# Performance work log

Hardware: AMD Instinct MI355X
Metric: run time of the kernel (lower is better)

## Reference

```python
import jax, jax.numpy as jnp
import numpy as np
import math

# --- static model config (mirrors FitTorch init args) ---
NATOMS = 2000
NNBR = 30            # neighbors per atom (regular neighlist)
NPAIRS = NATOMS * NNBR
NCONF = 8
APC = NATOMS // NCONF
NUM_RADIAL = 12
NUM_3BODY = 20
CUTOFF = 5.0
H1, H2 = 64, 32
DESC = NUM_RADIAL + NUM_3BODY


def setup_inputs() -> dict:
    key = jax.random.key(0)
    ks = jax.random.split(key, 12)
    # positions in a box
    x = jax.random.uniform(ks[0], (NATOMS, 3), jnp.float32, 0.0, 20.0)
    unique_i = jnp.repeat(jnp.arange(NATOMS, dtype=jnp.int32), NNBR)
    unique_j = jax.random.randint(ks[1], (NPAIRS,), 0, NATOMS, dtype=jnp.int32)
    # construct transform_x so every pair distance lies in (1.0, 0.95*cutoff)
    dirs = jax.random.normal(ks[2], (NPAIRS, 3), jnp.float32)
    dirs = dirs / jnp.linalg.norm(dirs, axis=1, keepdims=True)
    r = jax.random.uniform(ks[3], (NPAIRS, 1), jnp.float32, 1.0, 0.95 * CUTOFF)
    xneigh_target = x[unique_i] - dirs * r
    transform_x = xneigh_target - x[unique_j]
    neighlist = jnp.stack([unique_i, unique_j], axis=1)
    indices = unique_i // APC                      # config id per pair
    atoms_per_structure = jnp.full((NCONF,), APC, dtype=jnp.int32)
    types = jnp.zeros((NATOMS,), dtype=jnp.int32)
    # tiny pairwise MLP params (sigmoid hidden layers, linear output)
    def lin(k, fan_in, fan_out):
        return jax.random.normal(k, (fan_in, fan_out), jnp.float32) / np.sqrt(fan_in)
    W1 = lin(ks[4], DESC, H1); b1 = jnp.zeros((H1,), jnp.float32)
    W2 = lin(ks[5], H1, H2);   b2 = jnp.zeros((H2,), jnp.float32)
    W3 = lin(ks[6], H2, 1);    b3 = jnp.zeros((1,), jnp.float32)
    return {"x": x, "transform_x": transform_x, "neighlist": neighlist,
            "indices": indices, "atoms_per_structure": atoms_per_structure,
            "types": types, "unique_i": unique_i, "unique_j": unique_j,
            "W1": W1, "b1": b1, "W2": W2, "b2": b2, "W3": W3, "b3": b3}


def _energy(x, transform_x, indices, unique_i, unique_j, W1, b1, W2, b2, W3, b3, nconf):
    # gather + pairwise geometry
    xneigh = transform_x + x[unique_j]                      # [P,3]
    diff = x[unique_i] - xneigh                             # [P,3]
    rij = jnp.linalg.norm(diff, axis=1, keepdims=True)      # [P,1]
    u = diff / jnp.maximum(rij, 1e-12)                      # F.normalize
    # smooth cosine cutoff
    fc = 0.5 * (jnp.cos(jnp.pi * rij / CUTOFF) + 1.0)       # [P,1]
    # radial Bessel basis: fc * sqrt(2/c) * sin(n*pi*r/c) / r, n=1..R
    n = jnp.arange(1, NUM_RADIAL + 1, dtype=x.dtype)
    rbf = fc * jnp.sqrt(2.0 / CUTOFF) * jnp.sin(n * jnp.pi * rij / CUTOFF) / rij  # [P,R]
    # 3-body Gaussian descriptors over angles j-i-k (neighbors grouped per atom i)
    A, N, M = x.shape[0], NNBR, NUM_3BODY
    u3 = u.reshape(A, N, 3)
    fcn = fc.reshape(A, N)
    cos = jnp.einsum('apd,aqd->apq', u3, u3)                # [A,N,N] cos(theta)
    mu = jnp.linspace(-1.0, 1.0, M).astype(x.dtype)
    dmu = mu[1] - mu[0]
    eta = 1.0 / (2.0 * dmu * dmu)
    self_mask = 1.0 - jnp.eye(N, dtype=x.dtype)             # exclude k == j
    w = fcn[:, None, :] * self_mask[None]                   # [A,N,N] fc(r_ik) weights
    g = jnp.exp(-eta * (cos[..., None] - mu) ** 2)          # [A,N,N,M]
    d3 = jnp.einsum('apq,apqm->apm', w, g).reshape(A * N, M)
    # pairwise MLP -> pair energies, modulated by cutoff
    desc = jnp.concatenate([rbf, d3], axis=1)               # [P, DESC]
    h = jax.nn.sigmoid(desc @ W1 + b1)
    h = jax.nn.sigmoid(h @ W2 + b2)
    eij = (h @ W3 + b3) * fc                                # [P,1]
    # scatter pair energies to per-structure totals (index_add_)
    return jax.ops.segment_sum(eij[:, 0], indices, num_segments=nconf)


def reference(x, transform_x, neighlist, indices, atoms_per_structure, types,
              unique_i, unique_j, W1, b1, W2, b2, W3, b3):
    nconf = atoms_per_structure.shape[0]
    energy = _energy(x, transform_x, indices, unique_i, unique_j,
                     W1, b1, W2, b2, W3, b3, nconf)
    # forces = -d(sum of energies)/dx (grad_outputs = ones), as in torch.autograd.grad
    forces = -jax.grad(lambda xx: _energy(xx, transform_x, indices, unique_i, unique_j,
                                          W1, b1, W2, b2, W3, b3, nconf).sum())(x)
    return energy, forces
```

## Files before the change

kernel.cpp:

```cpp
#include <hip/hip_runtime.h>
#include <math.h>

#define NATOMS 2000
#define NNBR   30
#define NCONF  8
#define APC    250
#define NRAD   12
#define M3     20
#define H1N    64
#define H2N    32

#define MU(m) (-1.0f + (float)(m) * (2.0f / 19.0f))

typedef __attribute__((ext_vector_type(8))) short short8_t;
typedef __attribute__((ext_vector_type(4))) float f32x4;

__device__ __forceinline__ float sigmoidf(float v) {
    return 1.0f / (1.0f + __expf(-v));
}
__device__ __forceinline__ ushort f2bf(float f) {
    unsigned u = __float_as_uint(f);
    u += 0x7FFF + ((u >> 16) & 1);
    return (ushort)(u >> 16);
}
__device__ __forceinline__ float bf2f(ushort s) {
    return __uint_as_float(((unsigned)s) << 16);
}

extern "C" __global__ void __launch_bounds__(256)
fit_main(const float* __restrict__ x, const float* __restrict__ tx,
         const int* __restrict__ uj,
         const float* __restrict__ W1, const float* __restrict__ b1,
         const float* __restrict__ W2, const float* __restrict__ b2,
         const float* __restrict__ W3, const float* __restrict__ b3,
         float* __restrict__ gx, float* __restrict__ e_atom)
{
    const int tid  = threadIdx.x;
    const int lane = tid & 63;
    const int wid  = tid >> 6;
    const int atom = blockIdx.x;
    const int lr   = lane & 15;
    const int lg   = lane >> 4;

    __shared__ float  s_u[NNBR][4];
    __shared__ float  s_geo[NNBR][8];
    __shared__ int    s_j[NNBR];
    __shared__ __align__(16) float  s_desc[32 * 36];
    __shared__ __align__(16) ushort s_W1b[32 * 72];
    __shared__ __align__(16) ushort s_W2tb[32 * 72];
    __shared__ __align__(16) ushort s_h1b[32 * 72];
    __shared__ __align__(16) ushort s_gz2b[32 * 40];
    __shared__ __align__(16) float  s_gd[32 * 44];
    __shared__ float  s_outp[64];
    __shared__ float  s_red[32 * 5];

    const float k1  = 0.6283185307179586f;
    const float sq  = 0.6324555320336759f;
    const float eta = 45.125f;
    const float RHO = 0.36787944117144233f;
    const float C2  = -90.25f;

#pragma unroll
    for (int i = 0; i < 8; i++) {
        int idx = tid + 256 * i;
        s_W1b[(idx >> 6) * 72 + (idx & 63)] = f2bf(W1[idx]);
    }
#pragma unroll
    for (int i = 0; i < 8; i++) {
        int idx = tid + 256 * i;
        s_W2tb[(idx & 31) * 72 + (idx >> 5)] = f2bf(W2[idx]);
    }
    if (tid < NNBR) {
        int p = atom * NNBR + tid;
        int j = uj[p];
        float d0 = x[atom * 3 + 0] - x[j * 3 + 0] - tx[p * 3 + 0];
        float d1 = x[atom * 3 + 1] - x[j * 3 + 1] - tx[p * 3 + 1];
        float d2 = x[atom * 3 + 2] - x[j * 3 + 2] - tx[p * 3 + 2];
        float r = sqrtf(d0 * d0 + d1 * d1 + d2 * d2);
        float rinv = 1.0f / r;
        float sa, ca;
        __sincosf(k1 * r, &sa, &ca);
        float fc = 0.5f * (ca + 1.0f);
        s_u[tid][0] = d0 * rinv; s_u[tid][1] = d1 * rinv; s_u[tid][2] = d2 * rinv;
        s_geo[tid][0] = fc; s_geo[tid][1] = r; s_geo[tid][2] = rinv;
        s_geo[tid][3] = sa; s_geo[tid][4] = ca;
        s_j[tid] = j;
    }
    __syncthreads();

#pragma unroll 1
    for (int t = tid; t < NNBR * NRAD; t += 256) {
        int p = t / NRAD, n = t - p * NRAD;
        float s = __sinf((float)(n + 1) * k1 * s_geo[p][1]);
        s_desc[p * 36 + n] = s_geo[p][0] * sq * s * s_geo[p][2];
    }
    if (tid < 72) s_desc[30 * 36 + tid] = 0.f;
    if (tid < 240) {
        int p = tid >> 3, c = tid & 7;
        int q0 = (c < 6) ? 4 * c : 24 + 3 * (c - 6);
        int qn = (c < 6) ? 4 : 3;
        float up0 = s_u[p][0], up1 = s_u[p][1], up2 = s_u[p][2];
        float d3part[M3];
#pragma unroll
        for (int m = 0; m < M3; m++) d3part[m] = 0.f;
        for (int qq = 0; qq < qn; qq++) {
            int q = q0 + qq;
            float fq = (q == p) ? 0.f : s_geo[q][0];
            float cs = up0 * s_u[q][0] + up1 * s_u[q][1] + up2 * s_u[q][2];
            float E  = __expf(9.5f * cs);
            float Ei = __expf(-9.5f * cs);
            float t9 = cs - MU(9);
            float h9 = __expf(-eta * t9 * t9);
            float h = h9 * E, rr = E * RHO;
            d3part[10] = fmaf(fq, h, d3part[10]);
#pragma unroll
            for (int m = 11; m < 20; m++) {
                h *= rr; rr *= RHO;
                d3part[m] = fmaf(fq, h, d3part[m]);
            }
            h = h9; rr = RHO * Ei;
            d3part[9] = fmaf(fq, h, d3part[9]);
#pragma unroll
            for (int m = 8; m >= 0; m--) {
                h *= rr; rr *= RHO;
                d3part[m] = fmaf(fq, h, d3part[m]);
            }
        }
#pragma unroll
        for (int m = 0; m < M3; m++) {
            float v = d3part[m];
            v += __shfl_xor(v, 1);
            v += __shfl_xor(v, 2);
            v += __shfl_xor(v, 4);
            if (c == 0) s_desc[p * 36 + NRAD + m] = v;
        }
    }
    __syncthreads();

    {
        const int mt = wid & 1, ntb = (wid >> 1) * 2;
        short8_t a;
        {
            const float* dp = s_desc + (16 * mt + lr) * 36 + lg * 8;
            f32x4 v0 = *(const f32x4*)dp;
            f32x4 v1 = *(const f32x4*)(dp + 4);
            a[0] = (short)f2bf(v0[0]); a[1] = (short)f2bf(v0[1]);
            a[2] = (short)f2bf(v0[2]); a[3] = (short)f2bf(v0[3]);
            a[4] = (short)f2bf(v1[0]); a[5] = (short)f2bf(v1[1]);
            a[6] = (short)f2bf(v1[2]); a[7] = (short)f2bf(v1[3]);
        }
#pragma unroll
        for (int t = 0; t < 2; t++) {
            int nt = ntb + t;
            int col = 16 * nt + lr;
            short8_t b;
#pragma unroll
            for (int j = 0; j < 8; j++)
                b[j] = (short)s_W1b[(lg * 8 + j) * 72 + col];
            f32x4 c = {0.f, 0.f, 0.f, 0.f};
            c = __builtin_amdgcn_mfma_f32_16x16x32_bf16(a, b, c, 0, 0, 0);
            float b1v = b1[col];
#pragma unroll
            for (int rg = 0; rg < 4; rg++) {
                int p = 16 * mt + lg * 4 + rg;
                s_h1b[p * 72 + col] = f2bf(sigmoidf(c[rg] + b1v));
            }
        }
    }
    __syncthreads();

    {
        const int mt = wid & 1, nt = wid >> 1;
        f32x4 c = {0.f, 0.f, 0.f, 0.f};
#pragma unroll
        for (int kt = 0; kt < 2; kt++) {
            short8_t a = *(const short8_t*)&s_h1b[(16 * mt + lr) * 72 + kt * 32 + lg * 8];
            short8_t b = *(const short8_t*)&s_W2tb[(16 * nt + lr) * 72 + kt * 32 + lg * 8];
            c = __builtin_amdgcn_mfma_f32_16x16x32_bf16(a, b, c, 0, 0, 0);
        }
        int k2 = 16 * nt + lr;
        float b2v = b2[k2], w3v = W3[k2];
        float op[4];
#pragma unroll
        for (int rg = 0; rg < 4; rg++) {
            int p = 16 * mt + lg * 4 + rg;
            float s = sigmoidf(c[rg] + b2v);
            op[rg] = s * w3v;
            float g = (p < NNBR) ? s_geo[p][0] * w3v * s * (1.f - s) : 0.f;
            s_gz2b[p * 40 + k2] = f2bf(g);
        }
#pragma unroll
        for (int rg = 0; rg < 4; rg++) {
            op[rg] += __shfl_xor(op[rg], 1);
            op[rg] += __shfl_xor(op[rg], 2);
            op[rg] += __shfl_xor(op[rg], 4);
            op[rg] += __shfl_xor(op[rg], 8);
        }
        if (lr == 0) {
#pragma unroll
            for (int rg = 0; rg < 4; rg++)
                s_outp[nt * 32 + 16 * mt + lg * 4 + rg] = op[rg];
        }
    }
    __syncthreads();

    {
        const int mt = wid & 1, ntb = (wid >> 1) * 2;
        short8_t a = *(const short8_t*)&s_gz2b[(16 * mt + lr) * 40 + lg * 8];
#pragma unroll
        for (int t = 0; t < 2; t++) {
            int nt = ntb + t;
            int hcol = 16 * nt + lr;
            short8_t b;
#pragma unroll
            for (int j = 0; j < 8; j++)
                b[j] = (short)s_W2tb[(lg * 8 + j) * 72 + hcol];
            f32x4 c = {0.f, 0.f, 0.f, 0.f};
            c = __builtin_amdgcn_mfma_f32_16x16x32_bf16(a, b, c, 0, 0, 0);
#pragma unroll
            for (int rg = 0; rg < 4; rg++) {
                int p = 16 * mt + lg * 4 + rg;
                float hv = bf2f(s_h1b[p * 72 + hcol]);
                s_h1b[p * 72 + hcol] = f2bf(c[rg] * hv * (1.f - hv));
            }
        }
    }
    __syncthreads();

    {
        const int mt = wid & 1, nt = wid >> 1;
        f32x4 c = {0.f, 0.f, 0.f, 0.f};
#pragma unroll
        for (int kt = 0; kt < 2; kt++) {
            short8_t a = *(const short8_t*)&s_h1b[(16 * mt + lr) * 72 + kt * 32 + lg * 8];
            short8_t b = *(const short8_t*)&s_W1b[(16 * nt + lr) * 72 + kt * 32 + lg * 8];
            c = __builtin_amdgcn_mfma_f32_16x16x32_bf16(a, b, c, 0, 0, 0);
        }
        int d = 16 * nt + lr;
#pragma unroll
        for (int rg = 0; rg < 4; rg++)
            s_gd[(16 * mt + lg * 4 + rg) * 44 + d] = c[rg];
    }
    __syncthreads();

    if (tid < 240) {
        int p = tid >> 3, c = tid & 7;
        int q0 = (c < 6) ? 4 * c : 24 + 3 * (c - 6);
        int qn = (c < 6) ? 4 : 3;
        float up0 = s_u[p][0], up1 = s_u[p][1], up2 = s_u[p][2];
        float Ap[M3];
        {
            const f32x4* ap4 = (const f32x4*)(s_gd + p * 44 + NRAD);
#pragma unroll
            for (int t4 = 0; t4 < 5; t4++) {
                f32x4 v = ap4[t4];
                Ap[4 * t4 + 0] = v[0]; Ap[4 * t4 + 1] = v[1];
                Ap[4 * t4 + 2] = v[2]; Ap[4 * t4 + 3] = v[3];
            }
        }
        float fp_ = s_geo[p][0];
        float gu0 = 0.f, gu1 = 0.f, gu2 = 0.f, gfc = 0.f;
        for (int qq = 0; qq < qn; qq++) {
            int q = q0 + qq;
            float uq0 = s_u[q][0], uq1 = s_u[q][1], uq2 = s_u[q][2];
            float cs = up0 * uq0 + up1 * uq1 + up2 * uq2;
            float fq = s_geo[q][0];
            const float* Aq = s_gd + q * 44 + NRAD;
            float E  = __expf(9.5f * cs);
            float Ei = __expf(-9.5f * cs);
            float t9 = cs - MU(9);
            float h9 = __expf(-eta * t9 * t9);
            float sAde = 0.f, sBde = 0.f, sBh = 0.f;
            {
                float h = h9 * E, rr = E * RHO;
#pragma unroll
                for (int m = 10; m < 20; m++) {
                    if (m > 10) { h *= rr; rr *= RHO; }
                    float de = C2 * (cs - MU(m)) * h;
                    float aq = Aq[m];
                    sAde = fmaf(Ap[m], de, sAde);
                    sBde = fmaf(aq, de, sBde);
                    sBh  = fmaf(aq, h,  sBh);
                }
            }
            {
                float h = h9, rr = RHO * Ei;
#pragma unroll
                for (int m = 9; m >= 0; m--) {
                    if (m < 9) { h *= rr; rr *= RHO; }
                    float de = C2 * (cs - MU(m)) * h;
                    float aq = Aq[m];
                    sAde = fmaf(Ap[m], de, sAde);
                    sBde = fmaf(aq, de, sBde);
                    sBh  = fmaf(aq, h,  sBh);
                }
            }
            if (q != p) {
                float gcos = fq * sAde + fp_ * sBde;
                gu0 = fmaf(gcos, uq0, gu0);
                gu1 = fmaf(gcos, uq1, gu1);
                gu2 = fmaf(gcos, uq2, gu2);
                gfc += sBh;
            }
        }
        gu0 += __shfl_xor(gu0, 1); gu0 += __shfl_xor(gu0, 2); gu0 += __shfl_xor(gu0, 4);
        gu1 += __shfl_xor(gu1, 1); gu1 += __shfl_xor(gu1, 2); gu1 += __shfl_xor(gu1, 4);
        gu2 += __shfl_xor(gu2, 1); gu2 += __shfl_xor(gu2, 2); gu2 += __shfl_xor(gu2, 4);
        gfc += __shfl_xor(gfc, 1); gfc += __shfl_xor(gfc, 2); gfc += __shfl_xor(gfc, 4);
        if (c == 0) {
            s_red[p * 5 + 0] = gu0;
            s_red[p * 5 + 1] = gu1;
            s_red[p * 5 + 2] = gu2;
            s_red[p * 5 + 3] = gfc;
        }
    }
    __syncthreads();

    float gd0 = 0.f, gd1 = 0.f, gd2 = 0.f, eij = 0.f;
    if (tid < NNBR) {
        float fc = s_geo[tid][0], rinv = s_geo[tid][2];
        float sa = s_geo[tid][3], ca = s_geo[tid][4];
        float out = b3[0] + s_outp[tid] + s_outp[32 + tid];
        float u0 = s_u[tid][0], u1 = s_u[tid][1], u2 = s_u[tid][2];
        int j = s_j[tid];
        float grp = 0.f, gfp = 0.f;
        float sprev = 0.f, scur = sa, cprev = 1.f, ccur = ca;
#pragma unroll
        for (int d = 0; d < NRAD; d++) {
            float gdv = s_gd[tid * 44 + d];
            float n = (float)(d + 1);
            grp += gdv * fc * sq * rinv * (n * k1 * ccur - scur * rinv);
            gfp += gdv * sq * scur * rinv;
            float snext = 2.f * ca * scur - sprev; sprev = scur; scur = snext;
            float cnext = 2.f * ca * ccur - cprev; cprev = ccur; ccur = cnext;
        }
        float gfc = gfp + s_red[tid * 5 + 3] + out;
        float gu0 = s_red[tid * 5 + 0];
        float gu1 = s_red[tid * 5 + 1];
        float gu2 = s_red[tid * 5 + 2];
        float grf = grp + gfc * (-0.5f * k1 * sa);
        float gdot = gu0 * u0 + gu1 * u1 + gu2 * u2;
        gd0 = grf * u0 + (gu0 - gdot * u0) * rinv;
        gd1 = grf * u1 + (gu1 - gdot * u1) * rinv;
        gd2 = grf * u2 + (gu2 - gdot * u2) * rinv;
        atomicAdd(&gx[j * 3 + 0], -gd0);
        atomicAdd(&gx[j * 3 + 1], -gd1);
        atomicAdd(&gx[j * 3 + 2], -gd2);
        eij = out * fc;
    }
    if (wid == 0) {
#pragma unroll
        for (int off = 32; off > 0; off >>= 1) {
            gd0 += __shfl_xor(gd0, off);
            gd1 += __shfl_xor(gd1, off);
            gd2 += __shfl_xor(gd2, off);
            eij += __shfl_xor(eij, off);
        }
        if (tid == 0) {
            atomicAdd(&gx[atom * 3 + 0], gd0);
            atomicAdd(&gx[atom * 3 + 1], gd1);
            atomicAdd(&gx[atom * 3 + 2], gd2);
            e_atom[atom] = eij;
        }
    }
}

extern "C" __global__ void __launch_bounds__(256)
fit_finalize(const float* __restrict__ e_atom, const float* __restrict__ gx,
             float* __restrict__ out)
{
    int b = blockIdx.x;
    if (b < NCONF) {
        __shared__ float red[256];
        int t = threadIdx.x;
        red[t] = (t < APC) ? e_atom[b * APC + t] : 0.f;
        __syncthreads();
        for (int s = 128; s > 0; s >>= 1) {
            if (t < s) red[t] += red[t + s];
            __syncthreads();
        }
        if (t == 0) out[b] = red[0];
    } else {
        int idx = (b - NCONF) * 256 + threadIdx.x;
        if (idx < NATOMS * 3) out[NCONF + idx] = -gx[idx];
    }
}

extern "C" void kernel_launch(void* const* d_in, const int* in_sizes, int n_in,
                              void* d_out, int out_size, void* d_ws, size_t ws_size,
                              hipStream_t stream)
{
    const float* x  = (const float*)d_in[0];
    const float* tx = (const float*)d_in[1];
    const int*   uj = (const int*)d_in[7];
    const float* W1 = (const float*)d_in[8];
    const float* b1 = (const float*)d_in[9];
    const float* W2 = (const float*)d_in[10];
    const float* b2 = (const float*)d_in[11];
    const float* W3 = (const float*)d_in[12];
    const float* b3 = (const float*)d_in[13];

    float* gx     = (float*)d_ws;
    float* e_atom = gx + NATOMS * 3;

    hipMemsetAsync(gx, 0, NATOMS * 3 * sizeof(float), stream);

    fit_main<<<NATOMS, 256, 0, stream>>>(x, tx, uj, W1, b1, W2, b2, W3, b3,
                                         gx, e_atom);

    int fblocks = NCONF + (NATOMS * 3 + 255) / 256;
    fit_finalize<<<fblocks, 256, 0, stream>>>(e_atom, gx, (float*)d_out);
}
```

Baseline: 46.45 us.

## Store descriptor and transposed weights in bf16 for vector MFMA operand loads

```diff
diff --git a/kernel.cpp b/kernel.cpp
--- a/kernel.cpp
+++ b/kernel.cpp
@@ -45,12 +45,14 @@
     __shared__ float  s_u[NNBR][4];
     __shared__ float  s_geo[NNBR][8];
     __shared__ int    s_j[NNBR];
-    __shared__ __align__(16) float  s_desc[32 * 36];
-    __shared__ __align__(16) ushort s_W1b[32 * 72];
+    __shared__ __align__(16) ushort s_descb[32 * 40];
+    __shared__ __align__(16) ushort s_W1b [32 * 72];
+    __shared__ __align__(16) ushort s_W1tb[64 * 40];
     __shared__ __align__(16) ushort s_W2tb[32 * 72];
-    __shared__ __align__(16) ushort s_h1b[32 * 72];
+    __shared__ __align__(16) ushort s_W2b [64 * 40];
+    __shared__ __align__(16) ushort s_h1b [32 * 72];
     __shared__ __align__(16) ushort s_gz2b[32 * 40];
-    __shared__ __align__(16) float  s_gd[32 * 44];
+    __shared__ __align__(16) float  s_gd  [32 * 44];
     __shared__ float  s_outp[64];
     __shared__ float  s_red[32 * 5];
 
@@ -63,12 +65,18 @@
 #pragma unroll
     for (int i = 0; i < 8; i++) {
         int idx = tid + 256 * i;
-        s_W1b[(idx >> 6) * 72 + (idx & 63)] = f2bf(W1[idx]);
+        int d = idx >> 6, h = idx & 63;
+        ushort v = f2bf(W1[idx]);
+        s_W1b[d * 72 + h]  = v;
+        s_W1tb[h * 40 + d] = v;
     }
 #pragma unroll
     for (int i = 0; i < 8; i++) {
         int idx = tid + 256 * i;
-        s_W2tb[(idx & 31) * 72 + (idx >> 5)] = f2bf(W2[idx]);
+        int h = idx >> 5, k = idx & 31;
+        ushort v = f2bf(W2[idx]);
+        s_W2tb[k * 72 + h] = v;
+        s_W2b[h * 40 + k]  = v;
     }
     if (tid < NNBR) {
         int p = atom * NNBR + tid;
@@ -92,9 +100,9 @@
     for (int t = tid; t < NNBR * NRAD; t += 256) {
         int p = t / NRAD, n = t - p * NRAD;
         float s = __sinf((float)(n + 1) * k1 * s_geo[p][1]);
-        s_desc[p * 36 + n] = s_geo[p][0] * sq * s * s_geo[p][2];
-    }
-    if (tid < 72) s_desc[30 * 36 + tid] = 0.f;
+        s_descb[p * 40 + n] = f2bf(s_geo[p][0] * sq * s * s_geo[p][2]);
+    }
+    if (tid < 80) s_descb[30 * 40 + tid] = 0;
     if (tid < 240) {
         int p = tid >> 3, c = tid & 7;
         int q0 = (c < 6) ? 4 * c : 24 + 3 * (c - 6);
@@ -132,31 +140,18 @@
             v += __shfl_xor(v, 1);
             v += __shfl_xor(v, 2);
             v += __shfl_xor(v, 4);
-            if (c == 0) s_desc[p * 36 + NRAD + m] = v;
+            if (c == 0) s_descb[p * 40 + NRAD + m] = f2bf(v);
         }
     }
     __syncthreads();
 
     {
         const int mt = wid & 1, ntb = (wid >> 1) * 2;
-        short8_t a;
-        {
-            const float* dp = s_desc + (16 * mt + lr) * 36 + lg * 8;
-            f32x4 v0 = *(const f32x4*)dp;
-            f32x4 v1 = *(const f32x4*)(dp + 4);
-            a[0] = (short)f2bf(v0[0]); a[1] = (short)f2bf(v0[1]);
-            a[2] = (short)f2bf(v0[2]); a[3] = (short)f2bf(v0[3]);
-            a[4] = (short)f2bf(v1[0]); a[5] = (short)f2bf(v1[1]);
-            a[6] = (short)f2bf(v1[2]); a[7] = (short)f2bf(v1[3]);
-        }
+        short8_t a = *(const short8_t*)&s_descb[(16 * mt + lr) * 40 + lg * 8];
 #pragma unroll
         for (int t = 0; t < 2; t++) {
-            int nt = ntb + t;
-            int col = 16 * nt + lr;
-            short8_t b;
-#pragma unroll
-            for (int j = 0; j < 8; j++)
-                b[j] = (short)s_W1b[(lg * 8 + j) * 72 + col];
+            int col = 16 * (ntb + t) + lr;
+            short8_t b = *(const short8_t*)&s_W1tb[col * 40 + lg * 8];
             f32x4 c = {0.f, 0.f, 0.f, 0.f};
             c = __builtin_amdgcn_mfma_f32_16x16x32_bf16(a, b, c, 0, 0, 0);
             float b1v = b1[col];
@@ -209,12 +204,8 @@
         short8_t a = *(const short8_t*)&s_gz2b[(16 * mt + lr) * 40 + lg * 8];
 #pragma unroll
         for (int t = 0; t < 2; t++) {
-            int nt = ntb + t;
-            int hcol = 16 * nt + lr;
-            short8_t b;
-#pragma unroll
-            for (int j = 0; j < 8; j++)
-                b[j] = (short)s_W2tb[(lg * 8 + j) * 72 + hcol];
+            int hcol = 16 * (ntb + t) + lr;
+            short8_t b = *(const short8_t*)&s_W2b[hcol * 40 + lg * 8];
             f32x4 c = {0.f, 0.f, 0.f, 0.f};
             c = __builtin_amdgcn_mfma_f32_16x16x32_bf16(a, b, c, 0, 0, 0);
 #pragma unroll
@@ -265,22 +256,31 @@
             float uq0 = s_u[q][0], uq1 = s_u[q][1], uq2 = s_u[q][2];
             float cs = up0 * uq0 + up1 * uq1 + up2 * uq2;
             float fq = s_geo[q][0];
-            const float* Aq = s_gd + q * 44 + NRAD;
+            float Aq[M3];
+            {
+                const f32x4* aq4 = (const f32x4*)(s_gd + q * 44 + NRAD);
+#pragma unroll
+                for (int t4 = 0; t4 < 5; t4++) {
+                    f32x4 v = aq4[t4];
+                    Aq[4 * t4 + 0] = v[0]; Aq[4 * t4 + 1] = v[1];
+                    Aq[4 * t4 + 2] = v[2]; Aq[4 * t4 + 3] = v[3];
+                }
+            }
             float E  = __expf(9.5f * cs);
             float Ei = __expf(-9.5f * cs);
             float t9 = cs - MU(9);
             float h9 = __expf(-eta * t9 * t9);
-            float sAde = 0.f, sBde = 0.f, sBh = 0.f;
+            float SAh = 0.f, SAm = 0.f, SBh = 0.f, SBm = 0.f;
             {
                 float h = h9 * E, rr = E * RHO;
 #pragma unroll
                 for (int m = 10; m < 20; m++) {
                     if (m > 10) { h *= rr; rr *= RHO; }
-                    float de = C2 * (cs - MU(m)) * h;
-                    float aq = Aq[m];
-                    sAde = fmaf(Ap[m], de, sAde);
-                    sBde = fmaf(aq, de, sBde);
-                    sBh  = fmaf(aq, h,  sBh);
+                    float hm = MU(m) * h;
+                    SAh = fmaf(Ap[m], h,  SAh);
+                    SAm = fmaf(Ap[m], hm, SAm);
+                    SBh = fmaf(Aq[m], h,  SBh);
+                    SBm = fmaf(Aq[m], hm, SBm);
                 }
             }
             {
@@ -288,19 +288,19 @@
 #pragma unroll
                 for (int m = 9; m >= 0; m--) {
                     if (m < 9) { h *= rr; rr *= RHO; }
-                    float de = C2 * (cs - MU(m)) * h;
-                    float aq = Aq[m];
-                    sAde = fmaf(Ap[m], de, sAde);
-                    sBde = fmaf(aq, de, sBde);
-                    sBh  = fmaf(aq, h,  sBh);
+                    float hm = MU(m) * h;
+                    SAh = fmaf(Ap[m], h,  SAh);
+                    SAm = fmaf(Ap[m], hm, SAm);
+                    SBh = fmaf(Aq[m], h,  SBh);
+                    SBm = fmaf(Aq[m], hm, SBm);
                 }
             }
             if (q != p) {
-                float gcos = fq * sAde + fp_ * sBde;
+                float gcos = C2 * (fq * (cs * SAh - SAm) + fp_ * (cs * SBh - SBm));
                 gu0 = fmaf(gcos, uq0, gu0);
                 gu1 = fmaf(gcos, uq1, gu1);
                 gu2 = fmaf(gcos, uq2, gu2);
-                gfc += sBh;
+                gfc += SBh;
             }
         }
         gu0 += __shfl_xor(gu0, 1); gu0 += __shfl_xor(gu0, 2); gu0 += __shfl_xor(gu0, 4);
```

After: 50.01 us. 1.08x slower.
